# Optimization experiments

Hardware: AMD Instinct MI355X
Metric: run time of the kernel (lower is better)

## Reference

```python
import jax, jax.numpy as jnp
import numpy as np

B, S, D, Q, N, H = 2, 2048, 4096, 32, 8, 128
ROPE_THETA = 10000.0


def apply_rope(x, positions, head_dim, theta):
    # x: [B, S, heads, H], positions: [B, S] int
    half = head_dim // 2
    inv_freq = 1.0 / (theta ** (jnp.arange(half, dtype=jnp.float32) * 2.0 / head_dim))
    angles = positions.astype(jnp.float32)[..., None] * inv_freq  # [B, S, half]
    cos = jnp.cos(angles)[:, :, None, :]  # [B, S, 1, half]
    sin = jnp.sin(angles)[:, :, None, :]
    x1, x2 = x[..., :half], x[..., half:]
    return jnp.concatenate([x1 * cos - x2 * sin, x2 * cos + x1 * sin], axis=-1).astype(x.dtype)


def setup_inputs() -> dict:
    key = jax.random.key(0)
    ks = jax.random.split(key, 5)
    x = jax.random.normal(ks[0], (B, S, D), dtype=jnp.float32)
    positions = jnp.broadcast_to(jnp.arange(S, dtype=jnp.int32)[None, :], (B, S))
    scale = 0.02
    Wq = jax.random.normal(ks[1], (Q, D, H), dtype=jnp.float32) * scale
    Wk = jax.random.normal(ks[2], (N, D, H), dtype=jnp.float32) * scale
    Wv = jax.random.normal(ks[3], (N, D, H), dtype=jnp.float32) * scale
    Wo = jax.random.normal(ks[4], (Q, H, D), dtype=jnp.float32) * scale
    return {"x": x, "positions": positions, "Wq": Wq, "Wk": Wk, "Wv": Wv, "Wo": Wo}


def reference(x, positions, Wq, Wk, Wv, Wo):
    # Prefill path: QKV proj + RoPE + GQA causal attention + O proj.
    head_repeats = Q // N
    q_BSQH = jnp.einsum('BSD,QDH->BSQH', x, Wq)
    q_BSQH = apply_rope(q_BSQH, positions, H, ROPE_THETA)
    k_BSNH = jnp.einsum('BSD,NDH->BSNH', x, Wk)
    k_BSNH = apply_rope(k_BSNH, positions, H, ROPE_THETA)
    v_BSNH = jnp.einsum('BSD,NDH->BSNH', x, Wv)
    # GQA head repeat
    k_BTQH = jnp.repeat(k_BSNH, head_repeats, axis=2) if head_repeats > 1 else k_BSNH
    v_BTQH = jnp.repeat(v_BSNH, head_repeats, axis=2) if head_repeats > 1 else v_BSNH
    scores_BQST = jnp.einsum('BSQH,BTQH->BQST', q_BSQH, k_BTQH) / jnp.sqrt(jnp.float32(H))
    causal = jnp.tril(jnp.ones((1, 1, S, S), dtype=jnp.bool_))
    scores_BQST = jnp.where(causal, scores_BQST, -jnp.inf)
    weights_BQST = jax.nn.softmax(scores_BQST, axis=-1)
    out_BSQH = jnp.einsum('BQST,BTQH->BSQH', weights_BQST, v_BTQH)
    o_BSD = jnp.einsum('BSQH,QHD->BSD', out_BSQH, Wo)
    return o_BSD
```

## Files before the change

### kernel.cpp

```cpp
#include <hip/hip_runtime.h>
#include <cstdint>
#include <cstddef>

#define B_  2
#define S_  2048
#define D_  4096
#define QH_ 32
#define NH_ 8
#define HD_ 128
#define MROWS (B_ * S_)
#define NQKV  (QH_ * HD_ + 2 * NH_ * HD_)
#define KOFF  (QH_ * HD_)
#define VOFF  (QH_ * HD_ + NH_ * HD_)

typedef __attribute__((ext_vector_type(8))) short bf16x8;
typedef __attribute__((ext_vector_type(4))) float f32x4;

__device__ __forceinline__ unsigned short f2bf(float f) {
    unsigned int u = __float_as_uint(f);
    return (unsigned short)((u + 0x7FFFu + ((u >> 16) & 1u)) >> 16);
}
__device__ __forceinline__ float bf2f(unsigned short h) { return __uint_as_float(((unsigned int)h) << 16); }

__device__ __forceinline__ void gl2lds16(const void* g, void* l) {
    __builtin_amdgcn_global_load_lds(
        (const __attribute__((address_space(1))) void*)g,
        (__attribute__((address_space(3))) void*)l, 16, 0, 0);
}

__global__ __launch_bounds__(256)
void convert_bf16_kernel(const float* __restrict__ in, unsigned short* __restrict__ out)
{
    const size_t i = ((size_t)blockIdx.x * 256 + threadIdx.x) * 8;
    float4 a = *(const float4*)(in + i);
    float4 b = *(const float4*)(in + i + 4);
    uint4 o;
    o.x = (unsigned int)f2bf(a.x) | ((unsigned int)f2bf(a.y) << 16);
    o.y = (unsigned int)f2bf(a.z) | ((unsigned int)f2bf(a.w) << 16);
    o.z = (unsigned int)f2bf(b.x) | ((unsigned int)f2bf(b.y) << 16);
    o.w = (unsigned int)f2bf(b.z) | ((unsigned int)f2bf(b.w) << 16);
    *(uint4*)(out + i) = o;
}

__global__ __launch_bounds__(256)
void transpose_conv_kernel(const float* __restrict__ in, unsigned short* __restrict__ out,
                           int R, int C)
{
    __shared__ unsigned short tile[64][72];
    const int t  = threadIdx.x;
    const int c0 = blockIdx.x * 64;
    const int r0 = blockIdx.y * 64;
    in  += (size_t)blockIdx.z * R * C;
    out += (size_t)blockIdx.z * R * C;
    {
        const int rr = t >> 4;
        const int cc = (t & 15) * 4;
        #pragma unroll
        for (int p = 0; p < 4; ++p) {
            float4 v = *(const float4*)(in + (size_t)(r0 + p * 16 + rr) * C + c0 + cc);
            unsigned int lo = (unsigned int)f2bf(v.x) | ((unsigned int)f2bf(v.y) << 16);
            unsigned int hi = (unsigned int)f2bf(v.z) | ((unsigned int)f2bf(v.w) << 16);
            *(uint2*)&tile[p * 16 + rr][cc] = make_uint2(lo, hi);
        }
    }
    __syncthreads();
    {
        const int j  = t >> 3;
        const int i8 = (t & 7) * 8;
        #pragma unroll
        for (int p = 0; p < 2; ++p) {
            unsigned short tmp[8];
            #pragma unroll
            for (int e = 0; e < 8; ++e) tmp[e] = tile[i8 + e][p * 32 + j];
            *(uint4*)(out + (size_t)(c0 + p * 32 + j) * R + r0 + i8) = *(uint4*)tmp;
        }
    }
}

__global__ __launch_bounds__(256)
void transpose_v_kernel(const unsigned short* __restrict__ qkv, unsigned short* __restrict__ vt)
{
    __shared__ unsigned short tile[64][76];
    const int t  = threadIdx.x;
    const int z  = blockIdx.z;
    const int b  = z >> 3, kh = z & 7;
    const int h0 = blockIdx.x * 64;
    const int s0 = blockIdx.y * 64;
    const unsigned short* in = qkv + (size_t)(b * S_) * NQKV + VOFF + kh * HD_;
    unsigned short* outb = vt + (size_t)z * HD_ * S_;
    {
        const int rr = t >> 4;
        const int cc = (t & 15) * 4;
        #pragma unroll
        for (int p = 0; p < 4; ++p) {
            uint2 v = *(const uint2*)(in + (size_t)(s0 + p * 16 + rr) * NQKV + h0 + cc);
            *(uint2*)&tile[p * 16 + rr][cc] = v;
        }
    }
    __syncthreads();
    {
        const int j  = t >> 3;
        const int i8 = (t & 7) * 8;
        #pragma unroll
        for (int p = 0; p < 2; ++p) {
            unsigned short tmp[8];
            #pragma unroll
            for (int e = 0; e < 8; ++e) tmp[e] = tile[i8 + e][p * 32 + j];
            *(uint4*)(outb + (size_t)(h0 + p * 32 + j) * S_ + s0 + i8) = *(uint4*)tmp;
        }
    }
}

template<int CF32>
__global__ __launch_bounds__(512, 2)
void gemm256_kernel(const unsigned short* __restrict__ A,
                    const unsigned short* __restrict__ Bt,
                    void* __restrict__ Cp, int Nst, int K)
{
    __shared__ alignas(16) unsigned short lds[3][2][256][32];

    const int t = threadIdx.x, l = t & 63, w = t >> 6;
    const int gx  = gridDim.x;
    const int nwg = gx * gridDim.y;
    int lin = blockIdx.y * gx + blockIdx.x;
    lin = (lin & 7) * (nwg >> 3) + (lin >> 3);
    const int bn = (lin % gx) * 256, bm = (lin / gx) * 256;
    const int wr = w >> 2, wc = w & 3;
    const int lm = l & 15, lg = l >> 4;

    f32x4 acc[8][4];
    #pragma unroll
    for (int i = 0; i < 8; ++i)
        #pragma unroll
        for (int j = 0; j < 4; ++j) acc[i][j] = (f32x4){0.f, 0.f, 0.f, 0.f};

    const int srow = w * 16 + (l >> 2);
    const int scol = (l & 3) * 8;
    const unsigned short* Asrc = A  + (size_t)(bm + srow) * K + scol;
    const unsigned short* Bsrc = Bt + (size_t)(bn + srow) * K + scol;

    #define STAGE_A(tt, bb) do {                                                  \
        gl2lds16(Asrc + (size_t)(tt) * 32,                  &lds[bb][0][w*16][0]); \
        gl2lds16(Asrc + (size_t)128*K + (size_t)(tt) * 32,  &lds[bb][0][128 + w*16][0]); } while (0)
    #define STAGE_B(tt, bb) do {                                                  \
        gl2lds16(Bsrc + (size_t)(tt) * 32,                  &lds[bb][1][w*16][0]); \
        gl2lds16(Bsrc + (size_t)128*K + (size_t)(tt) * 32,  &lds[bb][1][128 + w*16][0]); } while (0)

    const int nkt = K >> 5;
    STAGE_A(0, 0); STAGE_B(0, 0);
    STAGE_A(1, 1); STAGE_B(1, 1);

    for (int kt = 0; kt < nkt; ++kt) {
        if (kt + 1 < nkt) asm volatile("s_waitcnt vmcnt(4)" ::: "memory");
        else              asm volatile("s_waitcnt vmcnt(0)" ::: "memory");
        asm volatile("s_barrier" ::: "memory");

        const unsigned short (*bufA)[32] = lds[kt % 3][0];
        const unsigned short (*bufB)[32] = lds[kt % 3][1];
        const int nb = (kt + 2) % 3;
        const bool pf = (kt + 2 < nkt);

        bf16x8 bfr[4], afr[4];
        #pragma unroll
        for (int j = 0; j < 4; ++j) bfr[j] = *(const bf16x8*)&bufB[wc * 64 + j * 16 + lm][lg * 8];
        #pragma unroll
        for (int i = 0; i < 4; ++i) afr[i] = *(const bf16x8*)&bufA[wr * 128 + i * 16 + lm][lg * 8];
        if (pf) STAGE_A(kt + 2, nb);
        #pragma unroll
        for (int i = 0; i < 4; ++i)
            #pragma unroll
            for (int j = 0; j < 4; ++j)
                acc[i][j] = __builtin_amdgcn_mfma_f32_16x16x32_bf16(afr[i], bfr[j], acc[i][j], 0, 0, 0);

        #pragma unroll
        for (int i = 0; i < 4; ++i) afr[i] = *(const bf16x8*)&bufA[wr * 128 + (i + 4) * 16 + lm][lg * 8];
        if (pf) STAGE_B(kt + 2, nb);
        #pragma unroll
        for (int i = 0; i < 4; ++i)
            #pragma unroll
            for (int j = 0; j < 4; ++j)
                acc[i + 4][j] = __builtin_amdgcn_mfma_f32_16x16x32_bf16(afr[i], bfr[j], acc[i + 4][j], 0, 0, 0);
    }
    #undef STAGE_A
    #undef STAGE_B

    const int lr4 = lg * 4;
    #pragma unroll
    for (int i = 0; i < 8; ++i) {
        #pragma unroll
        for (int j = 0; j < 4; ++j) {
            int row = bm + wr * 128 + i * 16 + lr4;
            int col = bn + wc * 64 + j * 16 + lm;
            #pragma unroll
            for (int jj = 0; jj < 4; ++jj) {
                if constexpr (CF32)
                    ((float*)Cp)[(size_t)(row + jj) * Nst + col] = acc[i][j][jj];
                else
                    ((unsigned short*)Cp)[(size_t)(row + jj) * Nst + col] = f2bf(acc[i][j][jj]);
            }
        }
    }
}

template<int LOG2H>
__global__ __launch_bounds__(256)
void rope_kernel(unsigned short* __restrict__ data, const int* __restrict__ positions)
{
    const int gid  = blockIdx.x * 256 + threadIdx.x;
    const int j    = gid & 63;
    const int hr   = gid >> 6;
    const int head = hr & ((1 << LOG2H) - 1);
    const int bs   = hr >> LOG2H;
    const float pos = (float)positions[bs];
    const float inv = expf(-0.14391156831f * (float)j);
    float s, c;
    sincosf(pos * inv, &s, &c);
    const size_t base = (size_t)bs * NQKV + head * HD_;
    const float x1 = bf2f(data[base + j]);
    const float x2 = bf2f(data[base + 64 + j]);
    data[base + j]      = f2bf(x1 * c - x2 * s);
    data[base + 64 + j] = f2bf(x2 * c + x1 * s);
}

__global__ __launch_bounds__(256)
void attn_kernel(const unsigned short* __restrict__ qkv,
                 const unsigned short* __restrict__ vt,
                 unsigned short* __restrict__ ao)
{
    constexpr int LDK = 136;
    constexpr int LDV = 72;
    __shared__ alignas(16) unsigned short k_s[64][LDK];
    __shared__ alignas(16) unsigned short v_t[128][LDV];
    __shared__ alignas(16) unsigned short p_s[4][16][LDV];

    const int t   = threadIdx.x;
    const int blk = blockIdx.x;
    const int sb  = 31 - (blk >> 6);
    const int pr  = blk & 63;
    const int qh  = pr >> 1;
    const int b   = pr & 1;
    const int kh  = qh >> 2;
    const int l   = t & 63, w = t >> 6;
    const int lm  = l & 15;
    const int lg  = l >> 4;
    const int lg4 = lg * 4;
    const int lko = lg * 8;
    const int wrow = w * 16 + lm;

    const unsigned short* vtb = vt + (size_t)(b * NH_ + kh) * HD_ * S_;

    bf16x8 qf[4];
    {
        const size_t qrow = (size_t)(b * S_ + sb * 64 + wrow) * NQKV + qh * HD_;
        #pragma unroll
        for (int kk = 0; kk < 4; ++kk)
            qf[kk] = *(const bf16x8*)(qkv + qrow + kk * 32 + lko);
    }

    f32x4 acc_o[8];
    #pragma unroll
    for (int i = 0; i < 8; ++i) acc_o[i] = (f32x4){0.f, 0.f, 0.f, 0.f};
    float mreg = -1e30f, lreg = 0.f;

    const float sm_scale = 0.08838834764831845f;

    for (int c = 0; c <= sb; ++c) {
        __syncthreads();
        {
            const int key = t >> 2, seg = t & 3;
            const size_t g = (size_t)(b * S_ + c * 64 + key) * NQKV + KOFF + kh * HD_ + seg * 32;
            const uint4* ksrc = (const uint4*)(qkv + g);
            #pragma unroll
            for (int i = 0; i < 4; ++i)
                *(uint4*)&k_s[key][seg * 32 + i * 8] = ksrc[i];
        }
        {
            const int h  = t >> 1;
            const int ko = (t & 1) * 32;
            const unsigned short* src = vtb + (size_t)h * S_ + c * 64 + ko;
            #pragma unroll
            for (int i = 0; i < 4; ++i)
                *(uint4*)&v_t[h][ko + i * 8] = *(const uint4*)(src + i * 8);
        }
        __syncthreads();

        f32x4 acc_s[4];
        #pragma unroll
        for (int t4 = 0; t4 < 4; ++t4) acc_s[t4] = (f32x4){0.f, 0.f, 0.f, 0.f};
        #pragma unroll
        for (int kk = 0; kk < 4; ++kk) {
            const bf16x8 qv = qf[kk];
            bf16x8 kf0 = *(const bf16x8*)&k_s[0 * 16 + lm][kk * 32 + lko];
            bf16x8 kf1 = *(const bf16x8*)&k_s[1 * 16 + lm][kk * 32 + lko];
            bf16x8 kf2 = *(const bf16x8*)&k_s[2 * 16 + lm][kk * 32 + lko];
            bf16x8 kf3 = *(const bf16x8*)&k_s[3 * 16 + lm][kk * 32 + lko];
            __builtin_amdgcn_s_setprio(1);
            acc_s[0] = __builtin_amdgcn_mfma_f32_16x16x32_bf16(kf0, qv, acc_s[0], 0, 0, 0);
            acc_s[1] = __builtin_amdgcn_mfma_f32_16x16x32_bf16(kf1, qv, acc_s[1], 0, 0, 0);
            acc_s[2] = __builtin_amdgcn_mfma_f32_16x16x32_bf16(kf2, qv, acc_s[2], 0, 0, 0);
            acc_s[3] = __builtin_amdgcn_mfma_f32_16x16x32_bf16(kf3, qv, acc_s[3], 0, 0, 0);
            __builtin_amdgcn_s_setprio(0);
        }

        const bool diag = (c == sb);
        float p[4][4];
        #pragma unroll
        for (int t4 = 0; t4 < 4; ++t4)
            #pragma unroll
            for (int r = 0; r < 4; ++r) {
                float s = acc_s[t4][r] * sm_scale;
                if (diag && (t4 * 16 + lg4 + r > wrow)) s = -1e30f;
                p[t4][r] = s;
            }
        float mc = p[0][0];
        #pragma unroll
        for (int t4 = 0; t4 < 4; ++t4)
            #pragma unroll
            for (int r = 0; r < 4; ++r) mc = fmaxf(mc, p[t4][r]);
        mc = fmaxf(mc, __shfl_xor(mc, 16, 64));
        mc = fmaxf(mc, __shfl_xor(mc, 32, 64));
        float sf = 1.0f;
        if (mc > mreg + 8.0f) {
            sf = __expf(mreg - mc);
            mreg = mc;
            lreg *= sf;
        }
        if (__any(sf != 1.0f)) {
            #pragma unroll
            for (int r = 0; r < 4; ++r) {
                const float s_r = __shfl(sf, (l & 48) | (lg4 + r), 64);
                #pragma unroll
                for (int ht = 0; ht < 8; ++ht) acc_o[ht][r] *= s_r;
            }
        }
        float ps = 0.f;
        #pragma unroll
        for (int t4 = 0; t4 < 4; ++t4)
            #pragma unroll
            for (int r = 0; r < 4; ++r) {
                p[t4][r] = __expf(p[t4][r] - mreg);
                ps += p[t4][r];
            }
        ps += __shfl_xor(ps, 16, 64);
        ps += __shfl_xor(ps, 32, 64);
        lreg += ps;
        #pragma unroll
        for (int t4 = 0; t4 < 4; ++t4) {
            unsigned int d0 = (unsigned int)f2bf(p[t4][0]) | ((unsigned int)f2bf(p[t4][1]) << 16);
            unsigned int d1 = (unsigned int)f2bf(p[t4][2]) | ((unsigned int)f2bf(p[t4][3]) << 16);
            *(unsigned int*)&p_s[w][lm][t4 * 16 + lg4]     = d0;
            *(unsigned int*)&p_s[w][lm][t4 * 16 + lg4 + 2] = d1;
        }

        #pragma unroll
        for (int kk = 0; kk < 2; ++kk) {
            const bf16x8 pa = *(const bf16x8*)&p_s[w][lm][kk * 32 + lko];
            #pragma unroll
            for (int ht = 0; ht < 8; ht += 4) {
                bf16x8 bv0 = *(const bf16x8*)&v_t[(ht + 0) * 16 + lm][kk * 32 + lko];
                bf16x8 bv1 = *(const bf16x8*)&v_t[(ht + 1) * 16 + lm][kk * 32 + lko];
                bf16x8 bv2 = *(const bf16x8*)&v_t[(ht + 2) * 16 + lm][kk * 32 + lko];
                bf16x8 bv3 = *(const bf16x8*)&v_t[(ht + 3) * 16 + lm][kk * 32 + lko];
                __builtin_amdgcn_s_setprio(1);
                acc_o[ht + 0] = __builtin_amdgcn_mfma_f32_16x16x32_bf16(pa, bv0, acc_o[ht + 0], 0, 0, 0);
                acc_o[ht + 1] = __builtin_amdgcn_mfma_f32_16x16x32_bf16(pa, bv1, acc_o[ht + 1], 0, 0, 0);
                acc_o[ht + 2] = __builtin_amdgcn_mfma_f32_16x16x32_bf16(pa, bv2, acc_o[ht + 2], 0, 0, 0);
                acc_o[ht + 3] = __builtin_amdgcn_mfma_f32_16x16x32_bf16(pa, bv3, acc_o[ht + 3], 0, 0, 0);
                __builtin_amdgcn_s_setprio(0);
            }
        }
    }

    #pragma unroll
    for (int r = 0; r < 4; ++r) {
        const float lr = __shfl(lreg, (l & 48) | (lg4 + r), 64);
        const float invl = 1.f / lr;
        const size_t row = (size_t)(b * S_ + sb * 64 + w * 16 + lg4 + r);
        #pragma unroll
        for (int ht = 0; ht < 8; ++ht)
            ao[(row * QH_ + qh) * HD_ + ht * 16 + lm] = f2bf(acc_o[ht][r] * invl);
    }
}

extern "C" void kernel_launch(void* const* d_in, const int* in_sizes, int n_in,
                              void* d_out, int out_size, void* d_ws, size_t ws_size,
                              hipStream_t stream)
{
    const float* x  = (const float*)d_in[0];
    const int*  pos = (const int*)d_in[1];
    const float* Wq = (const float*)d_in[2];
    const float* Wk = (const float*)d_in[3];
    const float* Wv = (const float*)d_in[4];
    const float* Wo = (const float*)d_in[5];
    float* out = (float*)d_out;

    char* wsb = (char*)d_ws;
    unsigned short* qkv = (unsigned short*)(wsb);
    unsigned short* wt  = (unsigned short*)(wsb + 50331648);
    unsigned short* vt  = (unsigned short*)(wsb + 83886080);
    unsigned short* r0  = (unsigned short*)(wsb + 100663296);

    const dim3 blk(256);
    const dim3 blk512(512);
    convert_bf16_kernel<<<8192, blk, 0, stream>>>(x, r0);
    transpose_conv_kernel<<<dim3(2, 64, 32), blk, 0, stream>>>(Wq, wt, D_, HD_);
    transpose_conv_kernel<<<dim3(2, 64, 8),  blk, 0, stream>>>(Wk, wt + (size_t)KOFF * D_, D_, HD_);
    transpose_conv_kernel<<<dim3(2, 64, 8),  blk, 0, stream>>>(Wv, wt + (size_t)VOFF * D_, D_, HD_);
    gemm256_kernel<0><<<dim3(NQKV / 256, MROWS / 256), blk512, 0, stream>>>(r0, wt, qkv, NQKV, D_);
    transpose_conv_kernel<<<dim3(64, 64, 1), blk, 0, stream>>>(Wo, wt, D_, D_);
    transpose_v_kernel<<<dim3(2, 32, 16), blk, 0, stream>>>(qkv, vt);
    rope_kernel<5><<<(MROWS * QH_ * 64) / 256, blk, 0, stream>>>(qkv, pos);
    rope_kernel<3><<<(MROWS * NH_ * 64) / 256, blk, 0, stream>>>(qkv + KOFF, pos);
    attn_kernel<<<B_ * QH_ * (S_ / 64), blk, 0, stream>>>(qkv, vt, r0);
    gemm256_kernel<1><<<dim3(D_ / 256, MROWS / 256), blk512, 0, stream>>>(r0, wt, out, D_, QH_ * HD_);
}
```

Measured before the change: 599.1 us.

## Double-buffer attention K/V tiles with direct global-to-LDS loads and swizzled layout

The attention kernel now keeps two LDS buffers for the K and V tiles. It prefetches the next 64-key chunk with direct global-to-LDS copies while the current chunk is being computed, which removes one barrier per iteration. The padded rows are replaced by an XOR/rotation-style swizzle so LDS stays bank-conflict free without padding. This doubles K/V shared-memory use, which may lower occupancy. Correctness depends on the async copies being complete before the single barrier at the top of each iteration.

```diff
diff --git a/kernel.cpp b/kernel.cpp
--- a/kernel.cpp
+++ b/kernel.cpp
@@ -227,11 +227,9 @@
                  const unsigned short* __restrict__ vt,
                  unsigned short* __restrict__ ao)
 {
-    constexpr int LDK = 136;
-    constexpr int LDV = 72;
-    __shared__ alignas(16) unsigned short k_s[64][LDK];
-    __shared__ alignas(16) unsigned short v_t[128][LDV];
-    __shared__ alignas(16) unsigned short p_s[4][16][LDV];
+    __shared__ alignas(16) unsigned short k_s[2][64][128];
+    __shared__ alignas(16) unsigned short v_t[2][128][64];
+    __shared__ alignas(16) unsigned short p_s[4][16][72];
 
     const int t   = threadIdx.x;
     const int blk = blockIdx.x;
@@ -246,8 +244,36 @@
     const int lg4 = lg * 4;
     const int lko = lg * 8;
     const int wrow = w * 16 + lm;
+    const int rot  = (lm & 7) * 8;
 
     const unsigned short* vtb = vt + (size_t)(b * NH_ + kh) * HD_ * S_;
+    const size_t kvrow0 = (size_t)(b * S_) * NQKV + KOFF + kh * HD_;
+
+    int ck[4], cv[2];
+    #pragma unroll
+    for (int kk = 0; kk < 4; ++kk) ck[kk] = (kk * 32 + lko - rot) & 127;
+    #pragma unroll
+    for (int kk = 0; kk < 2; ++kk) cv[kk] = (kk * 32 + lko - rot) & 63;
+
+    const int krsub = l >> 4, ksseg = (l & 15) * 8;
+    const int vrsub = l >> 3, vsseg = (l & 7) * 8;
+    #define STAGEKV(cc, bb) do {                                                   \
+        const int c64_ = (cc) * 64;                                                \
+        _Pragma("unroll")                                                          \
+        for (int i_ = 0; i_ < 4; ++i_) {                                           \
+            const int kr_ = w * 16 + i_ * 4 + krsub;                               \
+            const int ko_ = (ksseg + ((kr_ & 7) << 3)) & 127;                      \
+            gl2lds16(qkv + kvrow0 + (size_t)(c64_ + kr_) * NQKV + ko_,             \
+                     &k_s[bb][w * 16 + i_ * 4][0]);                                \
+        }                                                                          \
+        _Pragma("unroll")                                                          \
+        for (int i_ = 0; i_ < 4; ++i_) {                                           \
+            const int hv_ = w * 32 + i_ * 8 + vrsub;                               \
+            const int vo_ = (vsseg + ((hv_ & 7) << 3)) & 63;                       \
+            gl2lds16(vtb + (size_t)hv_ * S_ + c64_ + vo_,                          \
+                     &v_t[bb][w * 32 + i_ * 8][0]);                                \
+        }                                                                          \
+    } while (0)
 
     bf16x8 qf[4];
     {
@@ -264,25 +290,12 @@
 
     const float sm_scale = 0.08838834764831845f;
 
+    STAGEKV(0, 0);
+
     for (int c = 0; c <= sb; ++c) {
+        const int cur = c & 1;
         __syncthreads();
-        {
-            const int key = t >> 2, seg = t & 3;
-            const size_t g = (size_t)(b * S_ + c * 64 + key) * NQKV + KOFF + kh * HD_ + seg * 32;
-            const uint4* ksrc = (const uint4*)(qkv + g);
-            #pragma unroll
-            for (int i = 0; i < 4; ++i)
-                *(uint4*)&k_s[key][seg * 32 + i * 8] = ksrc[i];
-        }
-        {
-            const int h  = t >> 1;
-            const int ko = (t & 1) * 32;
-            const unsigned short* src = vtb + (size_t)h * S_ + c * 64 + ko;
-            #pragma unroll
-            for (int i = 0; i < 4; ++i)
-                *(uint4*)&v_t[h][ko + i * 8] = *(const uint4*)(src + i * 8);
-        }
-        __syncthreads();
+        if (c < sb) STAGEKV(c + 1, cur ^ 1);
 
         f32x4 acc_s[4];
         #pragma unroll
@@ -290,10 +303,10 @@
         #pragma unroll
         for (int kk = 0; kk < 4; ++kk) {
             const bf16x8 qv = qf[kk];
-            bf16x8 kf0 = *(const bf16x8*)&k_s[0 * 16 + lm][kk * 32 + lko];
-            bf16x8 kf1 = *(const bf16x8*)&k_s[1 * 16 + lm][kk * 32 + lko];
-            bf16x8 kf2 = *(const bf16x8*)&k_s[2 * 16 + lm][kk * 32 + lko];
-            bf16x8 kf3 = *(const bf16x8*)&k_s[3 * 16 + lm][kk * 32 + lko];
+            bf16x8 kf0 = *(const bf16x8*)&k_s[cur][0 * 16 + lm][ck[kk]];
+            bf16x8 kf1 = *(const bf16x8*)&k_s[cur][1 * 16 + lm][ck[kk]];
+            bf16x8 kf2 = *(const bf16x8*)&k_s[cur][2 * 16 + lm][ck[kk]];
+            bf16x8 kf3 = *(const bf16x8*)&k_s[cur][3 * 16 + lm][ck[kk]];
             __builtin_amdgcn_s_setprio(1);
             acc_s[0] = __builtin_amdgcn_mfma_f32_16x16x32_bf16(kf0, qv, acc_s[0], 0, 0, 0);
             acc_s[1] = __builtin_amdgcn_mfma_f32_16x16x32_bf16(kf1, qv, acc_s[1], 0, 0, 0);
@@ -357,10 +370,10 @@
             const bf16x8 pa = *(const bf16x8*)&p_s[w][lm][kk * 32 + lko];
             #pragma unroll
             for (int ht = 0; ht < 8; ht += 4) {
-                bf16x8 bv0 = *(const bf16x8*)&v_t[(ht + 0) * 16 + lm][kk * 32 + lko];
-                bf16x8 bv1 = *(const bf16x8*)&v_t[(ht + 1) * 16 + lm][kk * 32 + lko];
-                bf16x8 bv2 = *(const bf16x8*)&v_t[(ht + 2) * 16 + lm][kk * 32 + lko];
-                bf16x8 bv3 = *(const bf16x8*)&v_t[(ht + 3) * 16 + lm][kk * 32 + lko];
+                bf16x8 bv0 = *(const bf16x8*)&v_t[cur][(ht + 0) * 16 + lm][cv[kk]];
+                bf16x8 bv1 = *(const bf16x8*)&v_t[cur][(ht + 1) * 16 + lm][cv[kk]];
+                bf16x8 bv2 = *(const bf16x8*)&v_t[cur][(ht + 2) * 16 + lm][cv[kk]];
+                bf16x8 bv3 = *(const bf16x8*)&v_t[cur][(ht + 3) * 16 + lm][cv[kk]];
                 __builtin_amdgcn_s_setprio(1);
                 acc_o[ht + 0] = __builtin_amdgcn_mfma_f32_16x16x32_bf16(pa, bv0, acc_o[ht + 0], 0, 0, 0);
                 acc_o[ht + 1] = __builtin_amdgcn_mfma_f32_16x16x32_bf16(pa, bv1, acc_o[ht + 1], 0, 0, 0);
@@ -370,6 +383,7 @@
             }
         }
     }
+    #undef STAGEKV
 
     #pragma unroll
     for (int r = 0; r < 4; ++r) {
```

After: 584.3 us. -2.5%, faster.
